# Performance work log

Measured on AMD Instinct MI355X. Metric: run time of the kernel, lower is better.

The kernel has to match this reference:

```python
import jax, jax.numpy as jnp
import numpy as np

H = 1024           # hidden_size
E = 8              # num_experts
I = 4096 // E      # expert_intermediate_size = 512
V = 32000          # vocab_size
T = 4096           # num_tokens


def setup_inputs() -> dict:
    key = jax.random.key(0)
    ks = jax.random.split(key, 6)
    x = jax.random.normal(ks[0], (T, H), dtype=jnp.float32)
    token_ids = jax.random.randint(ks[1], (T,), 0, V, dtype=jnp.int64)
    mu = jax.random.normal(ks[2], (T, H), dtype=jnp.float32)
    # learned parameters (kaiming-like scale)
    gate_up_proj = jax.random.normal(ks[3], (E, H, 2 * I), dtype=jnp.float32) * (1.0 / np.sqrt(H))
    down_proj = jax.random.normal(ks[4], (E, I, H), dtype=jnp.float32) * (1.0 / np.sqrt(I))
    mu_w = jax.random.normal(ks[5], (E, H), dtype=jnp.float32) * 0.02  # mu_router.weight [E, H]
    return {"x": x, "token_ids": token_ids, "mu": mu,
            "gate_up_proj": gate_up_proj, "down_proj": down_proj, "mu_w": mu_w}


def reference(x, token_ids, mu, gate_up_proj, down_proj, mu_w):
    # deterministic base routing: expert = token_id % num_experts
    tid = jnp.clip(token_ids, 0, V - 1)
    base_expert = tid % E                                   # [T]
    # mu router biases the routing decision
    mu_logits = mu @ mu_w.T                                 # [T, E]
    combined = jax.nn.one_hot(base_expert, E, dtype=jnp.float32) * 10.0 + mu_logits
    expert_ids = jnp.argmax(combined, axis=-1)              # [T]

    out = jnp.zeros_like(x)
    # fixed small loop over experts; rows not routed to e are discarded by the mask,
    # so computing the dense GEMM over all tokens gives identical selected rows.
    for e in range(E):
        mask = (expert_ids == e)                            # [T]
        gu = x @ gate_up_proj[e]                            # [T, 2I]
        gate, up = gu[:, :I], gu[:, I:]
        inter = jax.nn.silu(gate) * up                      # [T, I]
        y = inter @ down_proj[e]                            # [T, H]
        out = jnp.where(mask[:, None], y, out)
    return out
```

## Files before the change

kernel.cpp:

```cpp
#include <hip/hip_runtime.h>
#include <cmath>

constexpr int T_DIM = 4096;
constexpr int H_DIM = 1024;
constexpr int E_DIM = 8;
constexpr int I_DIM = 512;
constexpr int V_DIM = 32000;

typedef _Float16 half_t;
typedef __attribute__((ext_vector_type(8))) _Float16 halfx8;
typedef __attribute__((ext_vector_type(4))) _Float16 halfx4;
typedef __attribute__((ext_vector_type(4))) float floatx4;

#define GLOAD16(g, l)                                                        \
    __builtin_amdgcn_global_load_lds(                                        \
        (const __attribute__((address_space(1))) void*)(g),                  \
        (__attribute__((address_space(3))) void*)(l), 16, 0, 0)

constexpr size_t OFF_COUNTS = 0;
constexpr size_t OFF_EID    = 1024;
constexpr size_t OFF_TOKL   = OFF_EID + (size_t)T_DIM * 4;
constexpr size_t OFF_XB     = OFF_TOKL + (size_t)E_DIM * T_DIM * 4;
constexpr size_t OFF_GUPT   = OFF_XB + (size_t)T_DIM * H_DIM * 2;
constexpr size_t OFF_DOWNT  = OFF_GUPT + (size_t)E_DIM * 2 * I_DIM * H_DIM * 2;
constexpr size_t OFF_INTER  = OFF_DOWNT + (size_t)E_DIM * H_DIM * I_DIM * 2;

__global__ __launch_bounds__(256) void route_logits_kernel(
    const float* __restrict__ mu, const int* __restrict__ token_ids,
    const float* __restrict__ mu_w, int* __restrict__ expert_id)
{
    const int t = blockIdx.x;
    const int tid = threadIdx.x;

    const float4 m = *(const float4*)&mu[(size_t)t * H_DIM + tid * 4];
    float acc[E_DIM];
#pragma unroll
    for (int e = 0; e < E_DIM; ++e) {
        const float4 w = *(const float4*)&mu_w[e * H_DIM + tid * 4];
        acc[e] = m.x * w.x + m.y * w.y + m.z * w.z + m.w * w.w;
    }
#pragma unroll
    for (int e = 0; e < E_DIM; ++e) {
#pragma unroll
        for (int off = 32; off > 0; off >>= 1)
            acc[e] += __shfl_down(acc[e], off, 64);
    }
    __shared__ float part[4][E_DIM];
    const int lane = tid & 63, w = tid >> 6;
    if (lane == 0) {
#pragma unroll
        for (int e = 0; e < E_DIM; ++e) part[w][e] = acc[e];
    }
    __syncthreads();
    if (tid == 0) {
        int tk = token_ids[t];
        tk = min(max(tk, 0), V_DIM - 1);
        const int be = tk & (E_DIM - 1);
        float best = -1e30f; int bi = 0;
#pragma unroll
        for (int e = 0; e < E_DIM; ++e) {
            const float c = part[0][e] + part[1][e] + part[2][e] + part[3][e]
                          + (e == be ? 10.f : 0.f);
            if (c > best) { best = c; bi = e; }
        }
        expert_id[t] = bi;
    }
}

__global__ __launch_bounds__(256) void prep_kernel(
    const float* __restrict__ x, const float* __restrict__ gup,
    const float* __restrict__ down, half_t* __restrict__ xb,
    half_t* __restrict__ gupT, half_t* __restrict__ downT,
    const int* __restrict__ expert_id, int* __restrict__ counts,
    int* __restrict__ tok_list)
{
    const int z = blockIdx.z, tid = threadIdx.x;

    if (z == 17) {
        if (blockIdx.x != 0 || blockIdx.y != 0) return;
        __shared__ int cnt[E_DIM];
        if (tid < E_DIM) cnt[tid] = 0;
        __syncthreads();
        for (int i = tid; i < T_DIM; i += 256) {
            const int e = expert_id[i];
            const int pos = atomicAdd(&cnt[e], 1);
            tok_list[e * T_DIM + pos] = i;
        }
        __syncthreads();
        if (tid < E_DIM) counts[tid] = cnt[tid];
        return;
    }

    if (z == 16) {
        const int blk = blockIdx.y * 16 + blockIdx.x;
#pragma unroll
        for (int p = 0; p < 16; ++p) {
            const size_t i = (size_t)blk * 16384 + p * 1024 + tid * 4;
            const float4 v = *(const float4*)&x[i];
            halfx4 h = { (half_t)v.x, (half_t)v.y, (half_t)v.z, (half_t)v.w };
            *(halfx4*)&xb[i] = h;
        }
        return;
    }

    __shared__ float tile[64][65];
    const float* se;  half_t* de;  int K;
    if (z < 8) {
        se = gup + (size_t)z * H_DIM * (2 * I_DIM);
        de = gupT + (size_t)z * (2 * I_DIM) * H_DIM;
        K = H_DIM;
    } else {
        if (blockIdx.y >= 8) return;
        const int e = z - 8;
        se = down + (size_t)e * I_DIM * H_DIM;
        de = downT + (size_t)e * H_DIM * I_DIM;
        K = I_DIM;
    }
    constexpr int N = 1024;
    const int n0 = blockIdx.x * 64, k0 = blockIdx.y * 64;
    const int c4 = (tid & 15) * 4, r0 = tid >> 4;
#pragma unroll
    for (int p = 0; p < 4; ++p) {
        const int r = r0 + p * 16;
        const float4 v = *(const float4*)&se[(size_t)(k0 + r) * N + n0 + c4];
        tile[r][c4 + 0] = v.x; tile[r][c4 + 1] = v.y;
        tile[r][c4 + 2] = v.z; tile[r][c4 + 3] = v.w;
    }
    __syncthreads();
#pragma unroll
    for (int p = 0; p < 4; ++p) {
        const int n = r0 + p * 16;
        const int kc = (tid & 15) * 4;
        halfx4 h = { (half_t)tile[kc + 0][n], (half_t)tile[kc + 1][n],
                     (half_t)tile[kc + 2][n], (half_t)tile[kc + 3][n] };
        *(halfx4*)&de[(size_t)(n0 + n) * K + k0 + kc] = h;
    }
}

__global__ __launch_bounds__(256) void gemm1_mfma_kernel(
    const half_t* __restrict__ xb, const half_t* __restrict__ gupT,
    const int* __restrict__ counts, const int* __restrict__ tok_list,
    half_t* __restrict__ inter)
{
    const int e = blockIdx.x;
    const int count = counts[e];
    const int m0 = blockIdx.z * 64;
    if (m0 >= count) return;
    const int n0 = blockIdx.y * 64;

    __shared__ __align__(16) half_t As[64 * 64];
    __shared__ __align__(16) half_t Bs[128 * 64];
    __shared__ int toks[64];

    const int tid = threadIdx.x;
    if (tid < 64) {
        const int m = m0 + tid;
        toks[tid] = (m < count) ? tok_list[e * T_DIM + m] : -1;
    }
    __syncthreads();

    const half_t* We = gupT + (size_t)e * (2 * I_DIM) * H_DIM;

    const int lane = tid & 63;
    const int w = tid >> 6;
    const int lr = lane >> 3, lc = lane & 7;

    const half_t* aptr[2]; const half_t* bptr[4];
    half_t *alds[2], *blds[4];
#pragma unroll
    for (int j = 0; j < 2; ++j) {
        const int r = w * 16 + j * 8 + lr;
        const int cg = lc ^ (r & 7);
        const int tk = toks[r];
        aptr[j] = xb + (size_t)(tk < 0 ? 0 : tk) * H_DIM + cg * 8;
        alds[j] = &As[(w * 16 + j * 8) * 64];
    }
#pragma unroll
    for (int j = 0; j < 4; ++j) {
        const int n = w * 32 + j * 8 + lr;
        const int col = (n < 64) ? (n0 + n) : (I_DIM + n0 + (n - 64));
        const int cg = lc ^ (n & 7);
        bptr[j] = We + (size_t)col * H_DIM + cg * 8;
        blds[j] = &Bs[(w * 32 + j * 8) * 64];
    }

    const floatx4 fzero = {0.f, 0.f, 0.f, 0.f};
    floatx4 accg[2][2], accu[2][2];
#pragma unroll
    for (int i = 0; i < 2; ++i)
#pragma unroll
        for (int j = 0; j < 2; ++j) { accg[i][j] = fzero; accu[i][j] = fzero; }

    const int wr = w >> 1, wc = w & 1;
    const int fm = lane & 15, q = lane >> 4;
    const int fm7 = fm & 7;

    for (int k0 = 0; k0 < H_DIM; k0 += 64) {
#pragma unroll
        for (int j = 0; j < 2; ++j) GLOAD16(aptr[j] + k0, alds[j]);
#pragma unroll
        for (int j = 0; j < 4; ++j) GLOAD16(bptr[j] + k0, blds[j]);
        __syncthreads();

#pragma unroll
        for (int ks = 0; ks < 2; ++ks) {
            const int swz = ((ks * 4 + q) ^ fm7) * 8;
            const halfx8 a0 = *(const halfx8*)&As[(32 * wr + fm) * 64 + swz];
            const halfx8 a1 = *(const halfx8*)&As[(32 * wr + 16 + fm) * 64 + swz];
#pragma unroll
            for (int ct = 0; ct < 2; ++ct) {
                const int ng = wc * 32 + ct * 16 + fm;
                const halfx8 bg = *(const halfx8*)&Bs[ng * 64 + swz];
                const halfx8 bu = *(const halfx8*)&Bs[(64 + ng) * 64 + swz];
                accg[0][ct] = __builtin_amdgcn_mfma_f32_16x16x32_f16(a0, bg, accg[0][ct], 0, 0, 0);
                accg[1][ct] = __builtin_amdgcn_mfma_f32_16x16x32_f16(a1, bg, accg[1][ct], 0, 0, 0);
                accu[0][ct] = __builtin_amdgcn_mfma_f32_16x16x32_f16(a0, bu, accu[0][ct], 0, 0, 0);
                accu[1][ct] = __builtin_amdgcn_mfma_f32_16x16x32_f16(a1, bu, accu[1][ct], 0, 0, 0);
            }
        }
        __syncthreads();
    }

#pragma unroll
    for (int rt = 0; rt < 2; ++rt)
#pragma unroll
        for (int r = 0; r < 4; ++r) {
            const int row = 32 * wr + 16 * rt + q * 4 + r;
            const int tk = toks[row];
            if (tk < 0) continue;
#pragma unroll
            for (int ct = 0; ct < 2; ++ct) {
                const float g = accg[rt][ct][r];
                const float u = accu[rt][ct][r];
                const float s = g / (1.f + __expf(-g)) * u;
                inter[(size_t)tk * I_DIM + n0 + wc * 32 + ct * 16 + fm] = (half_t)s;
            }
        }
}

__global__ __launch_bounds__(256) void gemm2_mfma_kernel(
    const half_t* __restrict__ inter, const half_t* __restrict__ downT,
    const int* __restrict__ counts, const int* __restrict__ tok_list,
    float* __restrict__ out)
{
    const int e = blockIdx.x;
    const int count = counts[e];
    const int m0 = blockIdx.z * 64;
    if (m0 >= count) return;
    const int n0 = blockIdx.y * 128;

    __shared__ __align__(16) half_t As[64 * 64];
    __shared__ __align__(16) half_t Bs[128 * 64];
    __shared__ int toks[64];

    const int tid = threadIdx.x;
    if (tid < 64) {
        const int m = m0 + tid;
        toks[tid] = (m < count) ? tok_list[e * T_DIM + m] : -1;
    }
    __syncthreads();

    const half_t* De = downT + (size_t)e * H_DIM * I_DIM;

    const int lane = tid & 63;
    const int w = tid >> 6;
    const int lr = lane >> 3, lc = lane & 7;

    const half_t* aptr[2]; const half_t* bptr[4];
    half_t *alds[2], *blds[4];
#pragma unroll
    for (int j = 0; j < 2; ++j) {
        const int r = w * 16 + j * 8 + lr;
        const int cg = lc ^ (r & 7);
        const int tk = toks[r];
        aptr[j] = inter + (size_t)(tk < 0 ? 0 : tk) * I_DIM + cg * 8;
        alds[j] = &As[(w * 16 + j * 8) * 64];
    }
#pragma unroll
    for (int j = 0; j < 4; ++j) {
        const int n = w * 32 + j * 8 + lr;
        const int cg = lc ^ (n & 7);
        bptr[j] = De + (size_t)(n0 + n) * I_DIM + cg * 8;
        blds[j] = &Bs[(w * 32 + j * 8) * 64];
    }

    const floatx4 fzero = {0.f, 0.f, 0.f, 0.f};
    floatx4 acc[2][4];
#pragma unroll
    for (int i = 0; i < 2; ++i)
#pragma unroll
        for (int j = 0; j < 4; ++j) acc[i][j] = fzero;

    const int wr = w >> 1, wc = w & 1;
    const int fm = lane & 15, q = lane >> 4;
    const int fm7 = fm & 7;

    for (int k0 = 0; k0 < I_DIM; k0 += 64) {
#pragma unroll
        for (int j = 0; j < 2; ++j) GLOAD16(aptr[j] + k0, alds[j]);
#pragma unroll
        for (int j = 0; j < 4; ++j) GLOAD16(bptr[j] + k0, blds[j]);
        __syncthreads();

#pragma unroll
        for (int ks = 0; ks < 2; ++ks) {
            const int swz = ((ks * 4 + q) ^ fm7) * 8;
            const halfx8 a0 = *(const halfx8*)&As[(32 * wr + fm) * 64 + swz];
            const halfx8 a1 = *(const halfx8*)&As[(32 * wr + 16 + fm) * 64 + swz];
#pragma unroll
            for (int ct = 0; ct < 4; ++ct) {
                const halfx8 b = *(const halfx8*)&Bs[(wc * 64 + ct * 16 + fm) * 64 + swz];
                acc[0][ct] = __builtin_amdgcn_mfma_f32_16x16x32_f16(a0, b, acc[0][ct], 0, 0, 0);
                acc[1][ct] = __builtin_amdgcn_mfma_f32_16x16x32_f16(a1, b, acc[1][ct], 0, 0, 0);
            }
        }
        __syncthreads();
    }

#pragma unroll
    for (int rt = 0; rt < 2; ++rt)
#pragma unroll
        for (int r = 0; r < 4; ++r) {
            const int row = 32 * wr + 16 * rt + q * 4 + r;
            const int tk = toks[row];
            if (tk < 0) continue;
#pragma unroll
            for (int ct = 0; ct < 4; ++ct)
                out[(size_t)tk * H_DIM + n0 + wc * 64 + ct * 16 + fm] = acc[rt][ct][r];
        }
}

extern "C" void kernel_launch(void* const* d_in, const int* in_sizes, int n_in,
                              void* d_out, int out_size, void* d_ws, size_t ws_size,
                              hipStream_t stream)
{
    const float* x         = (const float*)d_in[0];
    const int*   token_ids = (const int*)  d_in[1];
    const float* mu        = (const float*)d_in[2];
    const float* gup       = (const float*)d_in[3];
    const float* down      = (const float*)d_in[4];
    const float* mu_w      = (const float*)d_in[5];
    float* out = (float*)d_out;

    char* ws = (char*)d_ws;
    int*    counts    = (int*)(ws + OFF_COUNTS);
    int*    expert_id = (int*)(ws + OFF_EID);
    int*    tok_list  = (int*)(ws + OFF_TOKL);
    half_t* xb        = (half_t*)(ws + OFF_XB);
    half_t* gupT      = (half_t*)(ws + OFF_GUPT);
    half_t* downT     = (half_t*)(ws + OFF_DOWNT);
    half_t* inter     = (half_t*)(ws + OFF_INTER);

    route_logits_kernel<<<T_DIM, 256, 0, stream>>>(mu, token_ids, mu_w, expert_id);
    prep_kernel<<<dim3(16, 16, 18), 256, 0, stream>>>(
        x, gup, down, xb, gupT, downT, expert_id, counts, tok_list);
    gemm1_mfma_kernel<<<dim3(E_DIM, 8, T_DIM / 64), 256, 0, stream>>>(
        xb, gupT, counts, tok_list, inter);
    gemm2_mfma_kernel<<<dim3(E_DIM, 8, T_DIM / 64), 256, 0, stream>>>(
        inter, downT, counts, tok_list, out);
}
```

Baseline: 158.8 us.

## Use persistent-style grid-stride M tiles with 32-row tiles and 2-wave blocks

Both expert GEMMs shrink the per-block M tile from 64 to 32 rows and drop from four waves to two per block. The launch grid is fixed at 16 z-slices, and each block loops over M tiles with a stride of 512 instead of launching one block per 64-row tile and exiting early. This removes the many empty blocks launched for experts with few tokens and spreads uneven expert counts more evenly. In exchange, B-tile reuse per block is lower, there are more loads per thread, and each block runs serially through its M tiles with no prefetch overlap.

```diff
diff --git a/kernel.cpp b/kernel.cpp
--- a/kernel.cpp
+++ b/kernel.cpp
@@ -137,197 +137,197 @@
     }
 }
 
-__global__ __launch_bounds__(256) void gemm1_mfma_kernel(
+__global__ __launch_bounds__(128) void gemm1_mfma_kernel(
     const half_t* __restrict__ xb, const half_t* __restrict__ gupT,
     const int* __restrict__ counts, const int* __restrict__ tok_list,
     half_t* __restrict__ inter)
 {
     const int e = blockIdx.x;
     const int count = counts[e];
-    const int m0 = blockIdx.z * 64;
-    if (m0 >= count) return;
     const int n0 = blockIdx.y * 64;
 
-    __shared__ __align__(16) half_t As[64 * 64];
+    __shared__ __align__(16) half_t As[32 * 64];
     __shared__ __align__(16) half_t Bs[128 * 64];
-    __shared__ int toks[64];
+    __shared__ int toks[32];
 
     const int tid = threadIdx.x;
-    if (tid < 64) {
-        const int m = m0 + tid;
-        toks[tid] = (m < count) ? tok_list[e * T_DIM + m] : -1;
-    }
-    __syncthreads();
-
-    const half_t* We = gupT + (size_t)e * (2 * I_DIM) * H_DIM;
-
     const int lane = tid & 63;
     const int w = tid >> 6;
     const int lr = lane >> 3, lc = lane & 7;
-
-    const half_t* aptr[2]; const half_t* bptr[4];
-    half_t *alds[2], *blds[4];
-#pragma unroll
-    for (int j = 0; j < 2; ++j) {
-        const int r = w * 16 + j * 8 + lr;
-        const int cg = lc ^ (r & 7);
-        const int tk = toks[r];
-        aptr[j] = xb + (size_t)(tk < 0 ? 0 : tk) * H_DIM + cg * 8;
-        alds[j] = &As[(w * 16 + j * 8) * 64];
-    }
-#pragma unroll
-    for (int j = 0; j < 4; ++j) {
-        const int n = w * 32 + j * 8 + lr;
+    const int fm = lane & 15, q = lane >> 4;
+    const int fm7 = fm & 7;
+
+    const half_t* We = gupT + (size_t)e * (2 * I_DIM) * H_DIM;
+
+    const half_t* bptr[8];
+#pragma unroll
+    for (int j = 0; j < 8; ++j) {
+        const int n = w * 64 + j * 8 + lr;
         const int col = (n < 64) ? (n0 + n) : (I_DIM + n0 + (n - 64));
         const int cg = lc ^ (n & 7);
         bptr[j] = We + (size_t)col * H_DIM + cg * 8;
-        blds[j] = &Bs[(w * 32 + j * 8) * 64];
-    }
-
-    const floatx4 fzero = {0.f, 0.f, 0.f, 0.f};
-    floatx4 accg[2][2], accu[2][2];
-#pragma unroll
-    for (int i = 0; i < 2; ++i)
-#pragma unroll
-        for (int j = 0; j < 2; ++j) { accg[i][j] = fzero; accu[i][j] = fzero; }
-
-    const int wr = w >> 1, wc = w & 1;
-    const int fm = lane & 15, q = lane >> 4;
-    const int fm7 = fm & 7;
-
-    for (int k0 = 0; k0 < H_DIM; k0 += 64) {
-#pragma unroll
-        for (int j = 0; j < 2; ++j) GLOAD16(aptr[j] + k0, alds[j]);
-#pragma unroll
-        for (int j = 0; j < 4; ++j) GLOAD16(bptr[j] + k0, blds[j]);
-        __syncthreads();
-
-#pragma unroll
-        for (int ks = 0; ks < 2; ++ks) {
-            const int swz = ((ks * 4 + q) ^ fm7) * 8;
-            const halfx8 a0 = *(const halfx8*)&As[(32 * wr + fm) * 64 + swz];
-            const halfx8 a1 = *(const halfx8*)&As[(32 * wr + 16 + fm) * 64 + swz];
-#pragma unroll
-            for (int ct = 0; ct < 2; ++ct) {
-                const int ng = wc * 32 + ct * 16 + fm;
-                const halfx8 bg = *(const halfx8*)&Bs[ng * 64 + swz];
-                const halfx8 bu = *(const halfx8*)&Bs[(64 + ng) * 64 + swz];
-                accg[0][ct] = __builtin_amdgcn_mfma_f32_16x16x32_f16(a0, bg, accg[0][ct], 0, 0, 0);
-                accg[1][ct] = __builtin_amdgcn_mfma_f32_16x16x32_f16(a1, bg, accg[1][ct], 0, 0, 0);
-                accu[0][ct] = __builtin_amdgcn_mfma_f32_16x16x32_f16(a0, bu, accu[0][ct], 0, 0, 0);
-                accu[1][ct] = __builtin_amdgcn_mfma_f32_16x16x32_f16(a1, bu, accu[1][ct], 0, 0, 0);
+    }
+
+    for (int m0 = blockIdx.z * 32; m0 < count; m0 += 512) {
+        __syncthreads();
+        if (tid < 32) {
+            const int m = m0 + tid;
+            toks[tid] = (m < count) ? tok_list[e * T_DIM + m] : -1;
+        }
+        __syncthreads();
+
+        const half_t* aptr[2];
+#pragma unroll
+        for (int j = 0; j < 2; ++j) {
+            const int r = w * 16 + j * 8 + lr;
+            const int cg = lc ^ (r & 7);
+            const int tk = toks[r];
+            aptr[j] = xb + (size_t)(tk < 0 ? 0 : tk) * H_DIM + cg * 8;
+        }
+
+        const floatx4 fzero = {0.f, 0.f, 0.f, 0.f};
+        floatx4 accg[2][2], accu[2][2];
+#pragma unroll
+        for (int i = 0; i < 2; ++i)
+#pragma unroll
+            for (int j = 0; j < 2; ++j) { accg[i][j] = fzero; accu[i][j] = fzero; }
+
+        for (int k0 = 0; k0 < H_DIM; k0 += 64) {
+#pragma unroll
+            for (int j = 0; j < 2; ++j)
+                GLOAD16(aptr[j] + k0, &As[(w * 16 + j * 8) * 64]);
+#pragma unroll
+            for (int j = 0; j < 8; ++j)
+                GLOAD16(bptr[j] + k0, &Bs[(w * 64 + j * 8) * 64]);
+            __syncthreads();
+
+#pragma unroll
+            for (int ks = 0; ks < 2; ++ks) {
+                const int swz = ((ks * 4 + q) ^ fm7) * 8;
+                const halfx8 a0 = *(const halfx8*)&As[fm * 64 + swz];
+                const halfx8 a1 = *(const halfx8*)&As[(16 + fm) * 64 + swz];
+#pragma unroll
+                for (int ct = 0; ct < 2; ++ct) {
+                    const int ng = w * 32 + ct * 16 + fm;
+                    const halfx8 bg = *(const halfx8*)&Bs[ng * 64 + swz];
+                    const halfx8 bu = *(const halfx8*)&Bs[(64 + ng) * 64 + swz];
+                    accg[0][ct] = __builtin_amdgcn_mfma_f32_16x16x32_f16(a0, bg, accg[0][ct], 0, 0, 0);
+                    accg[1][ct] = __builtin_amdgcn_mfma_f32_16x16x32_f16(a1, bg, accg[1][ct], 0, 0, 0);
+                    accu[0][ct] = __builtin_amdgcn_mfma_f32_16x16x32_f16(a0, bu, accu[0][ct], 0, 0, 0);
+                    accu[1][ct] = __builtin_amdgcn_mfma_f32_16x16x32_f16(a1, bu, accu[1][ct], 0, 0, 0);
+                }
             }
-        }
-        __syncthreads();
-    }
-
-#pragma unroll
-    for (int rt = 0; rt < 2; ++rt)
-#pragma unroll
-        for (int r = 0; r < 4; ++r) {
-            const int row = 32 * wr + 16 * rt + q * 4 + r;
-            const int tk = toks[row];
-            if (tk < 0) continue;
-#pragma unroll
-            for (int ct = 0; ct < 2; ++ct) {
-                const float g = accg[rt][ct][r];
-                const float u = accu[rt][ct][r];
-                const float s = g / (1.f + __expf(-g)) * u;
-                inter[(size_t)tk * I_DIM + n0 + wc * 32 + ct * 16 + fm] = (half_t)s;
+            __syncthreads();
+        }
+
+#pragma unroll
+        for (int rt = 0; rt < 2; ++rt)
+#pragma unroll
+            for (int r = 0; r < 4; ++r) {
+                const int row = 16 * rt + q * 4 + r;
+                const int tk = toks[row];
+                if (tk < 0) continue;
+#pragma unroll
+                for (int ct = 0; ct < 2; ++ct) {
+                    const float g = accg[rt][ct][r];
+                    const float u = accu[rt][ct][r];
+                    const float s = g / (1.f + __expf(-g)) * u;
+                    inter[(size_t)tk * I_DIM + n0 + w * 32 + ct * 16 + fm] = (half_t)s;
+                }
             }
-        }
-}
-
-__global__ __launch_bounds__(256) void gemm2_mfma_kernel(
+    }
+}
+
+__global__ __launch_bounds__(128) void gemm2_mfma_kernel(
     const half_t* __restrict__ inter, const half_t* __restrict__ downT,
     const int* __restrict__ counts, const int* __restrict__ tok_list,
     float* __restrict__ out)
 {
     const int e = blockIdx.x;
     const int count = counts[e];
-    const int m0 = blockIdx.z * 64;
-    if (m0 >= count) return;
     const int n0 = blockIdx.y * 128;
 
-    __shared__ __align__(16) half_t As[64 * 64];
+    __shared__ __align__(16) half_t As[32 * 64];
     __shared__ __align__(16) half_t Bs[128 * 64];
-    __shared__ int toks[64];
+    __shared__ int toks[32];
 
     const int tid = threadIdx.x;
-    if (tid < 64) {
-        const int m = m0 + tid;
-        toks[tid] = (m < count) ? tok_list[e * T_DIM + m] : -1;
-    }
-    __syncthreads();
-
-    const half_t* De = downT + (size_t)e * H_DIM * I_DIM;
-
     const int lane = tid & 63;
     const int w = tid >> 6;
     const int lr = lane >> 3, lc = lane & 7;
-
-    const half_t* aptr[2]; const half_t* bptr[4];
-    half_t *alds[2], *blds[4];
-#pragma unroll
-    for (int j = 0; j < 2; ++j) {
-        const int r = w * 16 + j * 8 + lr;
-        const int cg = lc ^ (r & 7);
-        const int tk = toks[r];
-        aptr[j] = inter + (size_t)(tk < 0 ? 0 : tk) * I_DIM + cg * 8;
-        alds[j] = &As[(w * 16 + j * 8) * 64];
-    }
-#pragma unroll
-    for (int j = 0; j < 4; ++j) {
-        const int n = w * 32 + j * 8 + lr;
+    const int fm = lane & 15, q = lane >> 4;
+    const int fm7 = fm & 7;
+
+    const half_t* De = downT + (size_t)e * H_DIM * I_DIM;
+
+    const half_t* bptr[8];
+#pragma unroll
+    for (int j = 0; j < 8; ++j) {
+        const int n = w * 64 + j * 8 + lr;
         const int cg = lc ^ (n & 7);
         bptr[j] = De + (size_t)(n0 + n) * I_DIM + cg * 8;
-        blds[j] = &Bs[(w * 32 + j * 8) * 64];
-    }
-
-    const floatx4 fzero = {0.f, 0.f, 0.f, 0.f};
-    floatx4 acc[2][4];
-#pragma unroll
-    for (int i = 0; i < 2; ++i)
-#pragma unroll
-        for (int j = 0; j < 4; ++j) acc[i][j] = fzero;
-
-    const int wr = w >> 1, wc = w & 1;
-    const int fm = lane & 15, q = lane >> 4;
-    const int fm7 = fm & 7;
-
-    for (int k0 = 0; k0 < I_DIM; k0 += 64) {
-#pragma unroll
-        for (int j = 0; j < 2; ++j) GLOAD16(aptr[j] + k0, alds[j]);
-#pragma unroll
-        for (int j = 0; j < 4; ++j) GLOAD16(bptr[j] + k0, blds[j]);
-        __syncthreads();
-
-#pragma unroll
-        for (int ks = 0; ks < 2; ++ks) {
-            const int swz = ((ks * 4 + q) ^ fm7) * 8;
-            const halfx8 a0 = *(const halfx8*)&As[(32 * wr + fm) * 64 + swz];
-            const halfx8 a1 = *(const halfx8*)&As[(32 * wr + 16 + fm) * 64 + swz];
-#pragma unroll
-            for (int ct = 0; ct < 4; ++ct) {
-                const halfx8 b = *(const halfx8*)&Bs[(wc * 64 + ct * 16 + fm) * 64 + swz];
-                acc[0][ct] = __builtin_amdgcn_mfma_f32_16x16x32_f16(a0, b, acc[0][ct], 0, 0, 0);
-                acc[1][ct] = __builtin_amdgcn_mfma_f32_16x16x32_f16(a1, b, acc[1][ct], 0, 0, 0);
+    }
+
+    for (int m0 = blockIdx.z * 32; m0 < count; m0 += 512) {
+        __syncthreads();
+        if (tid < 32) {
+            const int m = m0 + tid;
+            toks[tid] = (m < count) ? tok_list[e * T_DIM + m] : -1;
+        }
+        __syncthreads();
+
+        const half_t* aptr[2];
+#pragma unroll
+        for (int j = 0; j < 2; ++j) {
+            const int r = w * 16 + j * 8 + lr;
+            const int cg = lc ^ (r & 7);
+            const int tk = toks[r];
+            aptr[j] = inter + (size_t)(tk < 0 ? 0 : tk) * I_DIM + cg * 8;
+        }
+
+        const floatx4 fzero = {0.f, 0.f, 0.f, 0.f};
+        floatx4 acc[2][4];
+#pragma unroll
+        for (int i = 0; i < 2; ++i)
+#pragma unroll
+            for (int j = 0; j < 4; ++j) acc[i][j] = fzero;
+
+        for (int k0 = 0; k0 < I_DIM; k0 += 64) {
+#pragma unroll
+            for (int j = 0; j < 2; ++j)
+                GLOAD16(aptr[j] + k0, &As[(w * 16 + j * 8) * 64]);
+#pragma unroll
+            for (int j = 0; j < 8; ++j)
+                GLOAD16(bptr[j] + k0, &Bs[(w * 64 + j * 8) * 64]);
+            __syncthreads();
+
+#pragma unroll
+            for (int ks = 0; ks < 2; ++ks) {
+                const int swz = ((ks * 4 + q) ^ fm7) * 8;
+                const halfx8 a0 = *(const halfx8*)&As[fm * 64 + swz];
+                const halfx8 a1 = *(const halfx8*)&As[(16 + fm) * 64 + swz];
+#pragma unroll
+                for (int ct = 0; ct < 4; ++ct) {
+                    const halfx8 b = *(const halfx8*)&Bs[(w * 64 + ct * 16 + fm) * 64 + swz];
+                    acc[0][ct] = __builtin_amdgcn_mfma_f32_16x16x32_f16(a0, b, acc[0][ct], 0, 0, 0);
+                    acc[1][ct] = __builtin_amdgcn_mfma_f32_16x16x32_f16(a1, b, acc[1][ct], 0, 0, 0);
+                }
             }
-        }
-        __syncthreads();
-    }
-
-#pragma unroll
-    for (int rt = 0; rt < 2; ++rt)
-#pragma unroll
-        for (int r = 0; r < 4; ++r) {
-            const int row = 32 * wr + 16 * rt + q * 4 + r;
-            const int tk = toks[row];
-            if (tk < 0) continue;
-#pragma unroll
-            for (int ct = 0; ct < 4; ++ct)
-                out[(size_t)tk * H_DIM + n0 + wc * 64 + ct * 16 + fm] = acc[rt][ct][r];
-        }
+            __syncthreads();
+        }
+
+#pragma unroll
+        for (int rt = 0; rt < 2; ++rt)
+#pragma unroll
+            for (int r = 0; r < 4; ++r) {
+                const int row = 16 * rt + q * 4 + r;
+                const int tk = toks[row];
+                if (tk < 0) continue;
+#pragma unroll
+                for (int ct = 0; ct < 4; ++ct)
+                    out[(size_t)tk * H_DIM + n0 + w * 64 + ct * 16 + fm] = acc[rt][ct][r];
+            }
+    }
 }
 
 extern "C" void kernel_launch(void* const* d_in, const int* in_sizes, int n_in,
@@ -354,8 +354,8 @@
     route_logits_kernel<<<T_DIM, 256, 0, stream>>>(mu, token_ids, mu_w, expert_id);
     prep_kernel<<<dim3(16, 16, 18), 256, 0, stream>>>(
         x, gup, down, xb, gupT, downT, expert_id, counts, tok_list);
-    gemm1_mfma_kernel<<<dim3(E_DIM, 8, T_DIM / 64), 256, 0, stream>>>(
+    gemm1_mfma_kernel<<<dim3(E_DIM, 8, 16), 128, 0, stream>>>(
         xb, gupT, counts, tok_list, inter);
-    gemm2_mfma_kernel<<<dim3(E_DIM, 8, T_DIM / 64), 256, 0, stream>>>(
+    gemm2_mfma_kernel<<<dim3(E_DIM, 8, 16), 128, 0, stream>>>(
         inter, downT, counts, tok_list, out);
 }
```

Result: slower. 175.2 us (+10.3%).

## Double-buffer LDS tiles and make MoE GEMM blocks persistent over M tiles

Applied to the files above, without the earlier changes.

Both expert GEMM kernels now double-buffer their A/B LDS tiles, prefetching the next K slice with global_load_lds while the current slice feeds MFMA. A partial vmcnt wait plus a raw s_barrier replaces the two full syncthreads per iteration. The grid's M dimension shrinks from 64 to 8 blocks, and each block loops over M tiles with stride 512, so far fewer blocks launch and then exit early. The price is twice the LDS, which may lower occupancy, and the last prefetch wraps around to load a redundant tile.

```diff
diff --git a/kernel.cpp b/kernel.cpp
--- a/kernel.cpp
+++ b/kernel.cpp
@@ -16,6 +16,9 @@
     __builtin_amdgcn_global_load_lds(                                        \
         (const __attribute__((address_space(1))) void*)(g),                  \
         (__attribute__((address_space(3))) void*)(l), 16, 0, 0)
+
+#define PIPE_BARRIER_WAIT6() asm volatile("s_waitcnt vmcnt(6)\n\ts_barrier" ::: "memory")
+#define PIPE_BARRIER()       asm volatile("s_barrier" ::: "memory")
 
 constexpr size_t OFF_COUNTS = 0;
 constexpr size_t OFF_EID    = 1024;
@@ -144,98 +147,114 @@
 {
     const int e = blockIdx.x;
     const int count = counts[e];
-    const int m0 = blockIdx.z * 64;
-    if (m0 >= count) return;
     const int n0 = blockIdx.y * 64;
 
-    __shared__ __align__(16) half_t As[64 * 64];
-    __shared__ __align__(16) half_t Bs[128 * 64];
+    __shared__ __align__(16) half_t As[2][64 * 64];
+    __shared__ __align__(16) half_t Bs[2][128 * 64];
     __shared__ int toks[64];
 
     const int tid = threadIdx.x;
-    if (tid < 64) {
-        const int m = m0 + tid;
-        toks[tid] = (m < count) ? tok_list[e * T_DIM + m] : -1;
-    }
-    __syncthreads();
-
-    const half_t* We = gupT + (size_t)e * (2 * I_DIM) * H_DIM;
-
     const int lane = tid & 63;
     const int w = tid >> 6;
     const int lr = lane >> 3, lc = lane & 7;
-
-    const half_t* aptr[2]; const half_t* bptr[4];
-    half_t *alds[2], *blds[4];
-#pragma unroll
-    for (int j = 0; j < 2; ++j) {
-        const int r = w * 16 + j * 8 + lr;
-        const int cg = lc ^ (r & 7);
-        const int tk = toks[r];
-        aptr[j] = xb + (size_t)(tk < 0 ? 0 : tk) * H_DIM + cg * 8;
-        alds[j] = &As[(w * 16 + j * 8) * 64];
-    }
+    const int wr = w >> 1, wc = w & 1;
+    const int fm = lane & 15, q = lane >> 4;
+    const int fm7 = fm & 7;
+
+    const half_t* We = gupT + (size_t)e * (2 * I_DIM) * H_DIM;
+
+    const half_t* bptr[4];
+    int blofs[4], alofs[2];
 #pragma unroll
     for (int j = 0; j < 4; ++j) {
         const int n = w * 32 + j * 8 + lr;
         const int col = (n < 64) ? (n0 + n) : (I_DIM + n0 + (n - 64));
         const int cg = lc ^ (n & 7);
         bptr[j] = We + (size_t)col * H_DIM + cg * 8;
-        blds[j] = &Bs[(w * 32 + j * 8) * 64];
-    }
-
-    const floatx4 fzero = {0.f, 0.f, 0.f, 0.f};
-    floatx4 accg[2][2], accu[2][2];
-#pragma unroll
-    for (int i = 0; i < 2; ++i)
-#pragma unroll
-        for (int j = 0; j < 2; ++j) { accg[i][j] = fzero; accu[i][j] = fzero; }
-
-    const int wr = w >> 1, wc = w & 1;
-    const int fm = lane & 15, q = lane >> 4;
-    const int fm7 = fm & 7;
-
-    for (int k0 = 0; k0 < H_DIM; k0 += 64) {
-#pragma unroll
-        for (int j = 0; j < 2; ++j) GLOAD16(aptr[j] + k0, alds[j]);
-#pragma unroll
-        for (int j = 0; j < 4; ++j) GLOAD16(bptr[j] + k0, blds[j]);
-        __syncthreads();
-
-#pragma unroll
-        for (int ks = 0; ks < 2; ++ks) {
-            const int swz = ((ks * 4 + q) ^ fm7) * 8;
-            const halfx8 a0 = *(const halfx8*)&As[(32 * wr + fm) * 64 + swz];
-            const halfx8 a1 = *(const halfx8*)&As[(32 * wr + 16 + fm) * 64 + swz];
-#pragma unroll
-            for (int ct = 0; ct < 2; ++ct) {
-                const int ng = wc * 32 + ct * 16 + fm;
-                const halfx8 bg = *(const halfx8*)&Bs[ng * 64 + swz];
-                const halfx8 bu = *(const halfx8*)&Bs[(64 + ng) * 64 + swz];
-                accg[0][ct] = __builtin_amdgcn_mfma_f32_16x16x32_f16(a0, bg, accg[0][ct], 0, 0, 0);
-                accg[1][ct] = __builtin_amdgcn_mfma_f32_16x16x32_f16(a1, bg, accg[1][ct], 0, 0, 0);
-                accu[0][ct] = __builtin_amdgcn_mfma_f32_16x16x32_f16(a0, bu, accu[0][ct], 0, 0, 0);
-                accu[1][ct] = __builtin_amdgcn_mfma_f32_16x16x32_f16(a1, bu, accu[1][ct], 0, 0, 0);
+        blofs[j] = (w * 32 + j * 8) * 64;
+    }
+#pragma unroll
+    for (int j = 0; j < 2; ++j) alofs[j] = (w * 16 + j * 8) * 64;
+
+    for (int m0 = blockIdx.z * 64; m0 < count; m0 += 512) {
+        __syncthreads();
+        if (tid < 64) {
+            const int m = m0 + tid;
+            toks[tid] = (m < count) ? tok_list[e * T_DIM + m] : -1;
+        }
+        __syncthreads();
+
+        const half_t* aptr[2];
+#pragma unroll
+        for (int j = 0; j < 2; ++j) {
+            const int r = w * 16 + j * 8 + lr;
+            const int cg = lc ^ (r & 7);
+            const int tk = toks[r];
+            aptr[j] = xb + (size_t)(tk < 0 ? 0 : tk) * H_DIM + cg * 8;
+        }
+
+        const floatx4 fzero = {0.f, 0.f, 0.f, 0.f};
+        floatx4 accg[2][2], accu[2][2];
+#pragma unroll
+        for (int i = 0; i < 2; ++i)
+#pragma unroll
+            for (int j = 0; j < 2; ++j) { accg[i][j] = fzero; accu[i][j] = fzero; }
+
+#pragma unroll
+        for (int j = 0; j < 2; ++j) GLOAD16(aptr[j], &As[0][alofs[j]]);
+#pragma unroll
+        for (int j = 0; j < 4; ++j) GLOAD16(bptr[j], &Bs[0][blofs[j]]);
+
+        int k0 = 0;
+        for (int it = 0; it < H_DIM / 64; ++it) {
+            const int kn = (k0 + 64) & (H_DIM - 1);
+            const int nb = (it + 1) & 1;
+#pragma unroll
+            for (int j = 0; j < 2; ++j) GLOAD16(aptr[j] + kn, &As[nb][alofs[j]]);
+#pragma unroll
+            for (int j = 0; j < 4; ++j) GLOAD16(bptr[j] + kn, &Bs[nb][blofs[j]]);
+
+            PIPE_BARRIER_WAIT6();
+
+            const half_t* Ac = As[it & 1];
+            const half_t* Bc = Bs[it & 1];
+#pragma unroll
+            for (int ks = 0; ks < 2; ++ks) {
+                const int swz = ((ks * 4 + q) ^ fm7) * 8;
+                const halfx8 a0 = *(const halfx8*)&Ac[(32 * wr + fm) * 64 + swz];
+                const halfx8 a1 = *(const halfx8*)&Ac[(32 * wr + 16 + fm) * 64 + swz];
+#pragma unroll
+                for (int ct = 0; ct < 2; ++ct) {
+                    const int ng = wc * 32 + ct * 16 + fm;
+                    const halfx8 bg = *(const halfx8*)&Bc[ng * 64 + swz];
+                    const halfx8 bu = *(const halfx8*)&Bc[(64 + ng) * 64 + swz];
+                    accg[0][ct] = __builtin_amdgcn_mfma_f32_16x16x32_f16(a0, bg, accg[0][ct], 0, 0, 0);
+                    accg[1][ct] = __builtin_amdgcn_mfma_f32_16x16x32_f16(a1, bg, accg[1][ct], 0, 0, 0);
+                    accu[0][ct] = __builtin_amdgcn_mfma_f32_16x16x32_f16(a0, bu, accu[0][ct], 0, 0, 0);
+                    accu[1][ct] = __builtin_amdgcn_mfma_f32_16x16x32_f16(a1, bu, accu[1][ct], 0, 0, 0);
+                }
             }
-        }
-        __syncthreads();
-    }
-
-#pragma unroll
-    for (int rt = 0; rt < 2; ++rt)
-#pragma unroll
-        for (int r = 0; r < 4; ++r) {
-            const int row = 32 * wr + 16 * rt + q * 4 + r;
-            const int tk = toks[row];
-            if (tk < 0) continue;
-#pragma unroll
-            for (int ct = 0; ct < 2; ++ct) {
-                const float g = accg[rt][ct][r];
-                const float u = accu[rt][ct][r];
-                const float s = g / (1.f + __expf(-g)) * u;
-                inter[(size_t)tk * I_DIM + n0 + wc * 32 + ct * 16 + fm] = (half_t)s;
+
+            PIPE_BARRIER();
+            k0 = kn;
+        }
+
+#pragma unroll
+        for (int rt = 0; rt < 2; ++rt)
+#pragma unroll
+            for (int r = 0; r < 4; ++r) {
+                const int row = 32 * wr + 16 * rt + q * 4 + r;
+                const int tk = toks[row];
+                if (tk < 0) continue;
+#pragma unroll
+                for (int ct = 0; ct < 2; ++ct) {
+                    const float g = accg[rt][ct][r];
+                    const float u = accu[rt][ct][r];
+                    const float s = g / (1.f + __expf(-g)) * u;
+                    inter[(size_t)tk * I_DIM + n0 + wc * 32 + ct * 16 + fm] = (half_t)s;
+                }
             }
-        }
+    }
 }
 
 __global__ __launch_bounds__(256) void gemm2_mfma_kernel(
@@ -245,89 +264,105 @@
 {
     const int e = blockIdx.x;
     const int count = counts[e];
-    const int m0 = blockIdx.z * 64;
-    if (m0 >= count) return;
     const int n0 = blockIdx.y * 128;
 
-    __shared__ __align__(16) half_t As[64 * 64];
-    __shared__ __align__(16) half_t Bs[128 * 64];
+    __shared__ __align__(16) half_t As[2][64 * 64];
+    __shared__ __align__(16) half_t Bs[2][128 * 64];
     __shared__ int toks[64];
 
     const int tid = threadIdx.x;
-    if (tid < 64) {
-        const int m = m0 + tid;
-        toks[tid] = (m < count) ? tok_list[e * T_DIM + m] : -1;
-    }
-    __syncthreads();
-
-    const half_t* De = downT + (size_t)e * H_DIM * I_DIM;
-
     const int lane = tid & 63;
     const int w = tid >> 6;
     const int lr = lane >> 3, lc = lane & 7;
-
-    const half_t* aptr[2]; const half_t* bptr[4];
-    half_t *alds[2], *blds[4];
-#pragma unroll
-    for (int j = 0; j < 2; ++j) {
-        const int r = w * 16 + j * 8 + lr;
-        const int cg = lc ^ (r & 7);
-        const int tk = toks[r];
-        aptr[j] = inter + (size_t)(tk < 0 ? 0 : tk) * I_DIM + cg * 8;
-        alds[j] = &As[(w * 16 + j * 8) * 64];
-    }
+    const int wr = w >> 1, wc = w & 1;
+    const int fm = lane & 15, q = lane >> 4;
+    const int fm7 = fm & 7;
+
+    const half_t* De = downT + (size_t)e * H_DIM * I_DIM;
+
+    const half_t* bptr[4];
+    int blofs[4], alofs[2];
 #pragma unroll
     for (int j = 0; j < 4; ++j) {
         const int n = w * 32 + j * 8 + lr;
         const int cg = lc ^ (n & 7);
         bptr[j] = De + (size_t)(n0 + n) * I_DIM + cg * 8;
-        blds[j] = &Bs[(w * 32 + j * 8) * 64];
-    }
-
-    const floatx4 fzero = {0.f, 0.f, 0.f, 0.f};
-    floatx4 acc[2][4];
-#pragma unroll
-    for (int i = 0; i < 2; ++i)
-#pragma unroll
-        for (int j = 0; j < 4; ++j) acc[i][j] = fzero;
-
-    const int wr = w >> 1, wc = w & 1;
-    const int fm = lane & 15, q = lane >> 4;
-    const int fm7 = fm & 7;
-
-    for (int k0 = 0; k0 < I_DIM; k0 += 64) {
-#pragma unroll
-        for (int j = 0; j < 2; ++j) GLOAD16(aptr[j] + k0, alds[j]);
-#pragma unroll
-        for (int j = 0; j < 4; ++j) GLOAD16(bptr[j] + k0, blds[j]);
-        __syncthreads();
-
-#pragma unroll
-        for (int ks = 0; ks < 2; ++ks) {
-            const int swz = ((ks * 4 + q) ^ fm7) * 8;
-            const halfx8 a0 = *(const halfx8*)&As[(32 * wr + fm) * 64 + swz];
-            const halfx8 a1 = *(const halfx8*)&As[(32 * wr + 16 + fm) * 64 + swz];
-#pragma unroll
-            for (int ct = 0; ct < 4; ++ct) {
-                const halfx8 b = *(const halfx8*)&Bs[(wc * 64 + ct * 16 + fm) * 64 + swz];
-                acc[0][ct] = __builtin_amdgcn_mfma_f32_16x16x32_f16(a0, b, acc[0][ct], 0, 0, 0);
-                acc[1][ct] = __builtin_amdgcn_mfma_f32_16x16x32_f16(a1, b, acc[1][ct], 0, 0, 0);
+        blofs[j] = (w * 32 + j * 8) * 64;
+    }
+#pragma unroll
+    for (int j = 0; j < 2; ++j) alofs[j] = (w * 16 + j * 8) * 64;
+
+    for (int m0 = blockIdx.z * 64; m0 < count; m0 += 512) {
+        __syncthreads();
+        if (tid < 64) {
+            const int m = m0 + tid;
+            toks[tid] = (m < count) ? tok_list[e * T_DIM + m] : -1;
+        }
+        __syncthreads();
+
+        const half_t* aptr[2];
+#pragma unroll
+        for (int j = 0; j < 2; ++j) {
+            const int r = w * 16 + j * 8 + lr;
+            const int cg = lc ^ (r & 7);
+            const int tk = toks[r];
+            aptr[j] = inter + (size_t)(tk < 0 ? 0 : tk) * I_DIM + cg * 8;
+        }
+
+        const floatx4 fzero = {0.f, 0.f, 0.f, 0.f};
+        floatx4 acc[2][4];
+#pragma unroll
+        for (int i = 0; i < 2; ++i)
+#pragma unroll
+            for (int j = 0; j < 4; ++j) acc[i][j] = fzero;
+
+#pragma unroll
+        for (int j = 0; j < 2; ++j) GLOAD16(aptr[j], &As[0][alofs[j]]);
+#pragma unroll
+        for (int j = 0; j < 4; ++j) GLOAD16(bptr[j], &Bs[0][blofs[j]]);
+
+        int k0 = 0;
+        for (int it = 0; it < I_DIM / 64; ++it) {
+            const int kn = (k0 + 64) & (I_DIM - 1);
+            const int nb = (it + 1) & 1;
+#pragma unroll
+            for (int j = 0; j < 2; ++j) GLOAD16(aptr[j] + kn, &As[nb][alofs[j]]);
+#pragma unroll
+            for (int j = 0; j < 4; ++j) GLOAD16(bptr[j] + kn, &Bs[nb][blofs[j]]);
+
+            PIPE_BARRIER_WAIT6();
+
+            const half_t* Ac = As[it & 1];
+            const half_t* Bc = Bs[it & 1];
+#pragma unroll
+            for (int ks = 0; ks < 2; ++ks) {
+                const int swz = ((ks * 4 + q) ^ fm7) * 8;
+                const halfx8 a0 = *(const halfx8*)&Ac[(32 * wr + fm) * 64 + swz];
+                const halfx8 a1 = *(const halfx8*)&Ac[(32 * wr + 16 + fm) * 64 + swz];
+#pragma unroll
+                for (int ct = 0; ct < 4; ++ct) {
+                    const halfx8 b = *(const halfx8*)&Bc[(wc * 64 + ct * 16 + fm) * 64 + swz];
+                    acc[0][ct] = __builtin_amdgcn_mfma_f32_16x16x32_f16(a0, b, acc[0][ct], 0, 0, 0);
+                    acc[1][ct] = __builtin_amdgcn_mfma_f32_16x16x32_f16(a1, b, acc[1][ct], 0, 0, 0);
+                }
             }
-        }
-        __syncthreads();
-    }
-
-#pragma unroll
-    for (int rt = 0; rt < 2; ++rt)
-#pragma unroll
-        for (int r = 0; r < 4; ++r) {
-            const int row = 32 * wr + 16 * rt + q * 4 + r;
-            const int tk = toks[row];
-            if (tk < 0) continue;
-#pragma unroll
-            for (int ct = 0; ct < 4; ++ct)
-                out[(size_t)tk * H_DIM + n0 + wc * 64 + ct * 16 + fm] = acc[rt][ct][r];
-        }
+
+            PIPE_BARRIER();
+            k0 = kn;
+        }
+
+#pragma unroll
+        for (int rt = 0; rt < 2; ++rt)
+#pragma unroll
+            for (int r = 0; r < 4; ++r) {
+                const int row = 32 * wr + 16 * rt + q * 4 + r;
+                const int tk = toks[row];
+                if (tk < 0) continue;
+#pragma unroll
+                for (int ct = 0; ct < 4; ++ct)
+                    out[(size_t)tk * H_DIM + n0 + wc * 64 + ct * 16 + fm] = acc[rt][ct][r];
+            }
+    }
 }
 
 extern "C" void kernel_launch(void* const* d_in, const int* in_sizes, int n_in,
@@ -354,8 +389,8 @@
     route_logits_kernel<<<T_DIM, 256, 0, stream>>>(mu, token_ids, mu_w, expert_id);
     prep_kernel<<<dim3(16, 16, 18), 256, 0, stream>>>(
         x, gup, down, xb, gupT, downT, expert_id, counts, tok_list);
-    gemm1_mfma_kernel<<<dim3(E_DIM, 8, T_DIM / 64), 256, 0, stream>>>(
+    gemm1_mfma_kernel<<<dim3(E_DIM, 8, 8), 256, 0, stream>>>(
         xb, gupT, counts, tok_list, inter);
-    gemm2_mfma_kernel<<<dim3(E_DIM, 8, T_DIM / 64), 256, 0, stream>>>(
+    gemm2_mfma_kernel<<<dim3(E_DIM, 8, 8), 256, 0, stream>>>(
         inter, downT, counts, tok_list, out);
 }
```

After: 172.9 us. 8.8% more time.
